# Performance work log

Measured on AMD Instinct MI355X. Metric: run time of the kernel, lower is better.

## Reference

```python
import math
import jax, jax.numpy as jnp
import numpy as np

L, H, D, DFF = 4, 8, 1024, 4096
RGB, AUD = 1024, 128
D_ATT, D_HOP, NCLS = 128, 4, 3862
B, T = 32, 300
EPS = 1e-6


def setup_inputs() -> dict:
    key = jax.random.key(0)
    ks = iter(jax.random.split(key, 40))
    s = 0.02
    p = {
        'padded_frame_rgbs': jax.random.uniform(next(ks), (B, T, RGB), jnp.float32),
        'padded_frame_audios': jax.random.uniform(next(ks), (B, T, AUD), jnp.float32),
        'embed_W': jax.random.normal(next(ks), (RGB + AUD, D), jnp.float32) * s,
        'embed_b': jnp.zeros((D,), jnp.float32),
        'Wq': jax.random.normal(next(ks), (L, D, D), jnp.float32) * s,
        'bq': jnp.zeros((L, D), jnp.float32),
        'Wk': jax.random.normal(next(ks), (L, D, D), jnp.float32) * s,
        'bk': jnp.zeros((L, D), jnp.float32),
        'Wv': jax.random.normal(next(ks), (L, D, D), jnp.float32) * s,
        'bv': jnp.zeros((L, D), jnp.float32),
        'Wo': jax.random.normal(next(ks), (L, D, D), jnp.float32) * s,
        'bo': jnp.zeros((L, D), jnp.float32),
        'ln1_a': jnp.ones((L, D), jnp.float32),
        'ln1_b': jnp.zeros((L, D), jnp.float32),
        'W1f': jax.random.normal(next(ks), (L, D, DFF), jnp.float32) * s,
        'b1f': jnp.zeros((L, DFF), jnp.float32),
        'W2f': jax.random.normal(next(ks), (L, DFF, D), jnp.float32) * s,
        'b2f': jnp.zeros((L, D), jnp.float32),
        'ln2_a': jnp.ones((L, D), jnp.float32),
        'ln2_b': jnp.zeros((L, D), jnp.float32),
        'fn_a': jnp.ones((D,), jnp.float32),
        'fn_b': jnp.zeros((D,), jnp.float32),
        'cw1': jax.random.normal(next(ks), (D, D_ATT), jnp.float32) * s,
        'cb1': jnp.zeros((D_ATT,), jnp.float32),
        'cw2': jax.random.normal(next(ks), (D_ATT, D_HOP), jnp.float32) * s,
        'cb2': jnp.zeros((D_HOP,), jnp.float32),
        'cw3': jax.random.normal(next(ks), (D_HOP * D, DFF), jnp.float32) * s,
        'cb3': jnp.zeros((DFF,), jnp.float32),
        'cw4': jax.random.normal(next(ks), (DFF, NCLS), jnp.float32) * s,
        'cb4': jnp.zeros((NCLS,), jnp.float32),
    }
    return p


def layernorm(x, a, b):
    # torch: a*(x-mean)/(std+eps)+b with unbiased std (ddof=1)
    mean = jnp.mean(x, axis=-1, keepdims=True)
    std = jnp.std(x, axis=-1, keepdims=True, ddof=1)
    return a * (x - mean) / (std + EPS) + b


def positional_encoding(T, D):
    pos = jnp.arange(T, dtype=jnp.float32)[:, None]
    div = jnp.exp(jnp.arange(0, D, 2, dtype=jnp.float32) * (-math.log(10000.0) / D))
    ang = pos * div  # [T, D/2]
    pe = jnp.stack([jnp.sin(ang), jnp.cos(ang)], axis=-1).reshape(T, D)
    return pe


def mha(x, Wq, bq, Wk, bk, Wv, bv, Wo, bo):
    dk = D // H
    q = (x @ Wq + bq).reshape(B, T, H, dk)
    k = (x @ Wk + bk).reshape(B, T, H, dk)
    v = (x @ Wv + bv).reshape(B, T, H, dk)
    scores = jnp.einsum('bthd,bshd->bhts', q, k) / math.sqrt(dk)
    p = jax.nn.softmax(scores, axis=-1)
    o = jnp.einsum('bhts,bshd->bthd', p, v).reshape(B, T, D)
    return o @ Wo + bo


def forward(padded_frame_rgbs, padded_frame_audios, embed_W, embed_b,
            Wq, bq, Wk, bk, Wv, bv, Wo, bo, ln1_a, ln1_b,
            W1f, b1f, W2f, b2f, ln2_a, ln2_b, fn_a, fn_b,
            cw1, cb1, cw2, cb2, cw3, cb3, cw4, cb4):
    feats = jnp.concatenate([padded_frame_rgbs / 255.0,
                             padded_frame_audios / 255.0], axis=2)
    x = (feats @ embed_W + embed_b) * math.sqrt(D)
    x = x + positional_encoding(T, D)[None]
    for i in range(L):
        x = x + mha(layernorm(x, ln1_a[i], ln1_b[i]),
                    Wq[i], bq[i], Wk[i], bk[i], Wv[i], bv[i], Wo[i], bo[i])
        h = layernorm(x, ln2_a[i], ln2_b[i])
        x = x + (jax.nn.relu(h @ W1f[i] + b1f[i]) @ W2f[i] + b2f[i])
    x = layernorm(x, fn_a, fn_b)
    # embedded classifier (multi-hop attention pooling)
    alpha = jnp.tanh(x @ cw1 + cb1) @ cw2 + cb2            # [B, T, D_HOP]
    alpha = jax.nn.softmax(alpha.transpose(0, 2, 1), -1)   # [B, D_HOP, T]
    ws = jnp.einsum('bht,btd->bhd', alpha, x).reshape(B, D_HOP * D)
    out = jnp.tanh(ws @ cw3 + cb3) @ cw4 + cb4             # [B, NCLS]
    return out, alpha


def reference(padded_frame_rgbs, padded_frame_audios, embed_W, embed_b,
              Wq, bq, Wk, bk, Wv, bv, Wo, bo, ln1_a, ln1_b,
              W1f, b1f, W2f, b2f, ln2_a, ln2_b, fn_a, fn_b,
              cw1, cb1, cw2, cb2, cw3, cb3, cw4, cb4):
    return forward(padded_frame_rgbs, padded_frame_audios, embed_W, embed_b,
                   Wq, bq, Wk, bk, Wv, bv, Wo, bo, ln1_a, ln1_b,
                   W1f, b1f, W2f, b2f, ln2_a, ln2_b, fn_a, fn_b,
                   cw1, cb1, cw2, cb2, cw3, cb3, cw4, cb4)
```

## Files before the change

kernel.cpp:

```cpp
#include <hip/hip_runtime.h>
#include <stdint.h>

#define NTOK 9600
#define TT   300
#define DD   1024
#define HH   8
#define DFF  4096
#define FIN  1152
#define DATT 128
#define NCLS 3862
#define TP   320
#define NQT  19

typedef unsigned short u16;
typedef __attribute__((ext_vector_type(8))) short short8;
typedef __attribute__((ext_vector_type(4))) float f32x4;

__device__ __forceinline__ int imin(int a, int b){ return a < b ? a : b; }

__device__ __forceinline__ u16 f2bf(float f){
    union { float f; uint32_t u; } v; v.f = f;
    uint32_t u = v.u;
    return (u16)((u + 0x7fffu + ((u >> 16) & 1u)) >> 16);
}

__device__ __forceinline__ f32x4 mfma16(short8 a, short8 b, f32x4 c){
    return __builtin_amdgcn_mfma_f32_16x16x32_bf16(a, b, c, 0, 0, 0);
}

__device__ __forceinline__ void gll16(const void* g, void* l){
    __builtin_amdgcn_global_load_lds((const __attribute__((address_space(1))) void*)g,
                                     (__attribute__((address_space(3))) void*)l, 16, 0, 0);
}

__global__ void __launch_bounds__(256) pe_kernel(float* __restrict__ pe)
{
    const int i = blockIdx.x * 256 + threadIdx.x;
    if (i >= TT * DD) return;
    const int t = i >> 10, d = i & 1023;
    const float fr = expf(-(float)(d & ~1) * (9.210340371976184f / 1024.0f));
    const float ang = (float)t * fr;
    pe[i] = (d & 1) ? cosf(ang) : sinf(ang);
}

__global__ void __launch_bounds__(256) feats_kernel(const float* __restrict__ rgb,
        const float* __restrict__ aud, u16* __restrict__ out)
{
    const long i = (long)blockIdx.x * 256 + threadIdx.x;
    if (i >= (long)NTOK * FIN) return;
    const int row = (int)(i / FIN), c = (int)(i % FIN);
    const float v = (c < 1024) ? rgb[(size_t)row * 1024 + c] : aud[(size_t)row * 128 + (c - 1024)];
    out[i] = f2bf(v * (1.0f / 255.0f));
}

__global__ void __launch_bounds__(256) wconv_kernel(const float* __restrict__ W,
        u16* __restrict__ Wt, int K, int N)
{
    __shared__ float tile[32][33];
    const int k0 = blockIdx.y * 32, n0 = blockIdx.x * 32;
    const int tx = threadIdx.x, ty = threadIdx.y;
    #pragma unroll
    for (int i = 0; i < 4; ++i) {
        const int k = k0 + ty + i * 8, n = n0 + tx;
        tile[ty + i * 8][tx] = (k < K && n < N) ? W[(size_t)k * N + n] : 0.f;
    }
    __syncthreads();
    #pragma unroll
    for (int i = 0; i < 4; ++i) {
        const int n = n0 + ty + i * 8, k = k0 + tx;
        if (n < N && k < K) Wt[(size_t)n * K + k] = f2bf(tile[tx][ty + i * 8]);
    }
}

__global__ void __launch_bounds__(256) wconv3_kernel(const float* __restrict__ W0,
        const float* __restrict__ W1, const float* __restrict__ W2, u16* __restrict__ Wt)
{
    __shared__ float tile[32][33];
    const float* W = (blockIdx.z == 0) ? W0 : ((blockIdx.z == 1) ? W1 : W2);
    u16* dst = Wt + (size_t)blockIdx.z * DD * DD;
    const int k0 = blockIdx.y * 32, n0 = blockIdx.x * 32;
    const int tx = threadIdx.x, ty = threadIdx.y;
    #pragma unroll
    for (int i = 0; i < 4; ++i)
        tile[ty + i * 8][tx] = W[(size_t)(k0 + ty + i * 8) * DD + n0 + tx];
    __syncthreads();
    #pragma unroll
    for (int i = 0; i < 4; ++i)
        dst[(size_t)(n0 + ty + i * 8) * DD + k0 + tx] = f2bf(tile[tx][ty + i * 8]);
}

__global__ void __launch_bounds__(256) f2bf_kernel(const float* __restrict__ in,
        u16* __restrict__ out, int n)
{
    const int i = blockIdx.x * 256 + threadIdx.x;
    if (i < n) out[i] = f2bf(in[i]);
}

__global__ void __launch_bounds__(256) qkvbias_kernel(const float* __restrict__ bq,
        const float* __restrict__ bk, const float* __restrict__ bv, float* __restrict__ out)
{
    const int i = blockIdx.x * 256 + threadIdx.x;
    if (i >= 4 * 3072) return;
    const int l = i / 3072, c = i % 3072;
    float v;
    if      (c < 1024) v = bq[l * 1024 + c];
    else if (c < 2048) v = bk[l * 1024 + c - 1024];
    else               v = bv[l * 1024 + c - 2048];
    out[i] = v;
}

template<int WF>
__global__ void __launch_bounds__(256) ln_kernel(const float* __restrict__ xin,
        const float* __restrict__ ga, const float* __restrict__ gb,
        u16* __restrict__ ob, float* of)
{
    const int row = blockIdx.x, t = threadIdx.x;
    const float4 xv = *(const float4*)(xin + (size_t)row * 1024 + t * 4);
    float s1 = xv.x + xv.y + xv.z + xv.w;
    float s2 = xv.x * xv.x + xv.y * xv.y + xv.z * xv.z + xv.w * xv.w;
    #pragma unroll
    for (int o = 1; o < 64; o <<= 1) { s1 += __shfl_xor(s1, o); s2 += __shfl_xor(s2, o); }
    __shared__ float r1[4], r2[4];
    const int lane = t & 63, wid = t >> 6;
    if (lane == 0) { r1[wid] = s1; r2[wid] = s2; }
    __syncthreads();
    s1 = r1[0] + r1[1] + r1[2] + r1[3];
    s2 = r2[0] + r2[1] + r2[2] + r2[3];
    const float mean = s1 * (1.0f / 1024.0f);
    const float var  = (s2 - 1024.0f * mean * mean) * (1.0f / 1023.0f);
    const float inv  = 1.0f / (sqrtf(fmaxf(var, 0.f)) + 1e-6f);
    const float4 av  = *(const float4*)(ga + t * 4);
    const float4 bv  = *(const float4*)(gb + t * 4);
    const float y0 = av.x * (xv.x - mean) * inv + bv.x;
    const float y1 = av.y * (xv.y - mean) * inv + bv.y;
    const float y2 = av.z * (xv.z - mean) * inv + bv.z;
    const float y3 = av.w * (xv.w - mean) * inv + bv.w;
    ushort4 o4; o4.x = f2bf(y0); o4.y = f2bf(y1); o4.z = f2bf(y2); o4.w = f2bf(y3);
    *(ushort4*)(ob + (size_t)row * 1024 + t * 4) = o4;
    if (WF) {
        float4 yo; yo.x = y0; yo.y = y1; yo.z = y2; yo.w = y3;
        *(float4*)(of + (size_t)row * 1024 + t * 4) = yo;
    }
}

#define EPI_EMBED        0
#define EPI_QKV          1
#define EPI_B_RELU_BF16  2
#define EPI_B_RES_F32    3
#define EPI_B_TANH_F32   4
#define EPI_ACC_F32      5
#define EPI_PART         6

template<int EPI, int SWZ>
__global__ void __launch_bounds__(256) gemm_k(const u16* __restrict__ A, const u16* __restrict__ Bt,
        const float* __restrict__ bias, const float* extra,
        float* outF, u16* outB, u16* outB2, u16* outB3, int M, int N, int K,
        int lda, int ldb, int kchunk)
{
    __shared__ __align__(16) u16 As[2][4096];
    __shared__ __align__(16) u16 Bs[2][4096];
    const int tid = threadIdx.x;
    int bm, bn;
    if (SWZ) {
        int lin = blockIdx.y * gridDim.x + blockIdx.x;
        const int nwg = gridDim.x * gridDim.y;
        const int cpx = nwg >> 3;
        lin = (lin & 7) * cpx + (lin >> 3);
        bm = lin / gridDim.x;
        bn = lin - bm * gridDim.x;
    } else {
        bm = blockIdx.y; bn = blockIdx.x;
    }
    const int lane = tid & 63, wid = tid >> 6;
    const int lg = lane >> 4, lr = lane & 15;
    const int wr = wid >> 1, wc = wid & 1;

    int koff = 0, Keff = K;
    if (kchunk > 0) { koff = blockIdx.z * kchunk; Keff = kchunk; }

    const int srow = tid >> 2;
    const int skc  = (tid & 3) * 8;
    const u16* ap0 = A  + (size_t)imin(bm * 128 + srow,      M - 1) * lda + skc + koff;
    const u16* ap1 = A  + (size_t)imin(bm * 128 + srow + 64, M - 1) * lda + skc + koff;
    const u16* bp0 = Bt + (size_t)imin(bn * 128 + srow,      N - 1) * ldb + skc + koff;
    const u16* bp1 = Bt + (size_t)imin(bn * 128 + srow + 64, N - 1) * ldb + skc + koff;

    f32x4 acc[4][4] = {};

    auto STAGE = [&](int b, int k0) {
        gll16(ap0 + k0, &As[b][tid * 8]);
        gll16(ap1 + k0, &As[b][2048 + tid * 8]);
        gll16(bp0 + k0, &Bs[b][tid * 8]);
        gll16(bp1 + k0, &Bs[b][2048 + tid * 8]);
    };
    auto COMPUTE = [&](int b) {
        short8 af[4], bf[4];
        #pragma unroll
        for (int m = 0; m < 4; ++m)
            af[m] = *(const short8*)(&As[b][(wr * 64 + m * 16 + lr) * 32 + lg * 8]);
        #pragma unroll
        for (int n = 0; n < 4; ++n)
            bf[n] = *(const short8*)(&Bs[b][(wc * 64 + n * 16 + lr) * 32 + lg * 8]);
        #pragma unroll
        for (int m = 0; m < 4; ++m)
            #pragma unroll
            for (int n = 0; n < 4; ++n)
                acc[m][n] = mfma16(af[m], bf[n], acc[m][n]);
    };

    STAGE(0, 0);
    __syncthreads();
    int cur = 0;
    for (int k0 = 32; k0 < Keff; k0 += 32) {
        STAGE(cur ^ 1, k0);
        COMPUTE(cur);
        __syncthreads();
        cur ^= 1;
    }
    COMPUTE(cur);

    #pragma unroll
    for (int m = 0; m < 4; ++m) {
        const int rb = bm * 128 + wr * 64 + m * 16 + lg * 4;
        #pragma unroll
        for (int n = 0; n < 4; ++n) {
            const int col = bn * 128 + wc * 64 + n * 16 + lr;
            if (col >= N) continue;
            const float bvl = (EPI == EPI_PART || EPI == EPI_ACC_F32) ? 0.f : bias[col];
            #pragma unroll
            for (int j = 0; j < 4; ++j) {
                const int r = rb + j;
                if (r >= M) continue;
                const float v = acc[m][n][j];
                const size_t oi = (size_t)r * N + col;
                if      (EPI == EPI_EMBED)       outF[oi] = (v + bvl) * 32.0f + extra[(size_t)(r % 300) * 1024 + col];
                else if (EPI == EPI_QKV) {
                    const int q = col >> 10, lc = col & 1023;
                    u16* dst = (q == 0) ? outB : ((q == 1) ? outB2 : outB3);
                    dst[(size_t)r * 1024 + lc] = f2bf(v + bvl);
                }
                else if (EPI == EPI_B_RELU_BF16) outB[oi] = f2bf(fmaxf(v + bvl, 0.f));
                else if (EPI == EPI_B_RES_F32)   outF[oi] = v + bvl + extra[oi];
                else if (EPI == EPI_B_TANH_F32)  outF[oi] = tanhf(v + bvl);
                else if (EPI == EPI_ACC_F32)     outF[oi] = v + extra[oi];
                else if (EPI == EPI_PART)        outF[(size_t)blockIdx.z * M * N + oi] = v;
            }
        }
    }
}

template<int EPI>
__global__ void __launch_bounds__(512, 2) gemm_big(const u16* __restrict__ A, const u16* __restrict__ Bt,
        const float* __restrict__ bias, const float* __restrict__ extra,
        float* outF, u16* outB, u16* outB2, u16* outB3,
        int M, int N, int K, int lda, int ldb, int kchunk)
{
    __shared__ __align__(16) u16 LA[2][256 * 32];
    __shared__ __align__(16) u16 LB[2][256 * 32];
    const int tid = threadIdx.x;
    int lin = blockIdx.x;
    const int nwg = gridDim.x;
    if ((nwg & 7) == 0) { const int cpx = nwg >> 3; lin = (lin & 7) * cpx + (lin >> 3); }
    int z = 0;
    if (kchunk > 0) { z = lin & 1; lin >>= 1; }
    const int ntN = N >> 8;
    const int bm = lin / ntN, bn = lin - (lin / ntN) * ntN;
    const int koff = z * kchunk;
    const int Keff = (kchunk > 0) ? kchunk : K;

    const int lane = tid & 63, wid = tid >> 6;
    const int wm = wid >> 2, wn = wid & 3;
    const int lg = lane >> 4, lr = lane & 15;

    const int prow = tid >> 2;
    const int skg  = (((tid & 3) ^ ((tid >> 3) & 3)) * 8);
    const u16* asrc0 = A  + (size_t)imin(bm * 256 + prow,       M - 1) * lda + skg + koff;
    const u16* asrc1 = A  + (size_t)imin(bm * 256 + prow + 128, M - 1) * lda + skg + koff;
    const u16* bsrc0 = Bt + (size_t)(bn * 256 + prow)       * ldb + skg + koff;
    const u16* bsrc1 = Bt + (size_t)(bn * 256 + prow + 128) * ldb + skg + koff;

    auto STAGE = [&](int s, int k0) {
        gll16(asrc0 + k0, &LA[s][tid * 8]);
        gll16(asrc1 + k0, &LA[s][4096 + tid * 8]);
        gll16(bsrc0 + k0, &LB[s][tid * 8]);
        gll16(bsrc1 + k0, &LB[s][4096 + tid * 8]);
    };

    const int kge = (lg ^ ((lr >> 1) & 3)) * 8;
    int aoff[8], boff[4];
    #pragma unroll
    for (int m = 0; m < 8; ++m) aoff[m] = (wm * 128 + m * 16 + lr) * 32 + kge;
    #pragma unroll
    for (int n = 0; n < 4; ++n) boff[n] = (wn * 64 + n * 16 + lr) * 32 + kge;

    f32x4 acc[8][4] = {};
    short8 af[8], bf[4];

    const int nk = Keff >> 5;
    STAGE(0, 0);
    STAGE(1, 32);
    asm volatile("s_waitcnt vmcnt(4)" ::: "memory");
    asm volatile("s_barrier" ::: "memory");
    __builtin_amdgcn_sched_barrier(0);

    auto BODY = [&](int t, int s, bool doStage) {
        #pragma unroll
        for (int m = 0; m < 8; ++m) af[m] = *(const short8*)(&LA[s][aoff[m]]);
        #pragma unroll
        for (int n = 0; n < 4; ++n) bf[n] = *(const short8*)(&LB[s][boff[n]]);
        asm volatile("s_waitcnt lgkmcnt(0)" ::: "memory");
        __builtin_amdgcn_sched_barrier(0);
        __builtin_amdgcn_s_setprio(1);
        #pragma unroll
        for (int m = 0; m < 4; ++m)
            #pragma unroll
            for (int n = 0; n < 4; ++n)
                acc[m][n] = mfma16(af[m], bf[n], acc[m][n]);
        __builtin_amdgcn_s_setprio(0);
        asm volatile("s_barrier" ::: "memory");
        __builtin_amdgcn_sched_barrier(0);
        if (doStage) STAGE(s, (t + 2) * 32);
        __builtin_amdgcn_s_setprio(1);
        #pragma unroll
        for (int m = 4; m < 8; ++m)
            #pragma unroll
            for (int n = 0; n < 4; ++n)
                acc[m][n] = mfma16(af[m], bf[n], acc[m][n]);
        __builtin_amdgcn_s_setprio(0);
    };

    for (int t = 0; t < nk - 2; ++t) {
        BODY(t, t & 1, true);
        asm volatile("s_waitcnt vmcnt(4)" ::: "memory");
        __builtin_amdgcn_sched_barrier(0);
        asm volatile("s_barrier" ::: "memory");
        __builtin_amdgcn_sched_barrier(0);
    }
    BODY(nk - 2, (nk - 2) & 1, false);
    asm volatile("s_waitcnt vmcnt(0)" ::: "memory");
    __builtin_amdgcn_sched_barrier(0);
    asm volatile("s_barrier" ::: "memory");
    __builtin_amdgcn_sched_barrier(0);
    BODY(nk - 1, (nk - 1) & 1, false);

    #pragma unroll
    for (int m = 0; m < 8; ++m) {
        const int rb = bm * 256 + wm * 128 + m * 16 + lg * 4;
        #pragma unroll
        for (int n = 0; n < 4; ++n) {
            const int col = bn * 256 + wn * 64 + n * 16 + lr;
            const float bvl = (EPI == EPI_PART) ? 0.f : bias[col];
            #pragma unroll
            for (int j = 0; j < 4; ++j) {
                const int r = rb + j;
                if (r >= M) continue;
                const float v = acc[m][n][j] + bvl;
                const size_t oi = (size_t)r * N + col;
                if (EPI == EPI_QKV) {
                    const int q = col >> 10, lc = col & 1023;
                    u16* dst = (q == 0) ? outB : ((q == 1) ? outB2 : outB3);
                    dst[(size_t)r * 1024 + lc] = f2bf(v);
                }
                else if (EPI == EPI_B_RELU_BF16) outB[oi] = f2bf(fmaxf(v, 0.f));
                else if (EPI == EPI_B_RES_F32)   outF[oi] = v + extra[oi];
                else if (EPI == EPI_EMBED)       outF[oi] = v * 32.0f + extra[(size_t)(r % 300) * 1024 + col];
                else if (EPI == EPI_PART)        outF[(size_t)z * M * N + oi] = v;
            }
        }
    }
}

template<int TANH>
__global__ void __launch_bounds__(256) redk_kernel(const float* __restrict__ part,
        const float* __restrict__ bias, float* outF, u16* outB, int M, int N, int Z)
{
    const int i = blockIdx.x * 256 + threadIdx.x;
    if (i >= M * N) return;
    const int col = i % N;
    float s = 0.f;
    for (int z = 0; z < Z; ++z) s += part[(size_t)z * M * N + i];
    s += bias[col];
    if (TANH) outB[i] = f2bf(tanhf(s));
    else      outF[i] = s;
}

__global__ void __launch_bounds__(512) attn_scores_kernel(const u16* __restrict__ Qb,
        const u16* __restrict__ Kb, u16* __restrict__ P)
{
    __shared__ __align__(16) u16 Ks[304 * 128];
    __shared__ __align__(16) u16 Ps[8][16][TP];
    const int bh = blockIdx.x, b = bh >> 3, h = bh & 7;
    const int tid = threadIdx.x, lane = tid & 63, wid = tid >> 6;
    const int lg = lane >> 4, lr = lane & 15;

    for (int c = tid; c < 304 * 16; c += 512) {
        const int kv = c >> 4, part = c & 15;
        const int tok = b * 300 + imin(kv, 299);
        const short8 v = *(const short8*)(Kb + (size_t)tok * 1024 + h * 128 + part * 8);
        int byte_ = kv * 256 + part * 16;
        byte_ ^= (kv & 7) << 4;
        *(short8*)((char*)Ks + byte_) = v;
    }
    __syncthreads();

    const float scale = 0.08838834764831845f;
    for (int qt = wid; qt < NQT; qt += 8) {
        f32x4 acc[NQT] = {};
        const int qtok = b * 300 + imin(qt * 16 + lr, 299);
        const u16* qrow = Qb + (size_t)qtok * 1024 + h * 128;
        #pragma unroll
        for (int kk = 0; kk < 4; ++kk) {
            const short8 aq = *(const short8*)(qrow + kk * 32 + lg * 8);
            #pragma unroll
            for (int nt = 0; nt < NQT; ++nt) {
                const int kvrow = nt * 16 + lr;
                int byte_ = kvrow * 256 + kk * 64 + lg * 16;
                byte_ ^= (kvrow & 7) << 4;
                const short8 bk = *(const short8*)((char*)Ks + byte_);
                acc[nt] = mfma16(aq, bk, acc[nt]);
            }
        }
        const int sw = lg << 3;
        #pragma unroll
        for (int j = 0; j < 4; ++j) {
            float vals[NQT];
            float m = -1e30f;
            #pragma unroll
            for (int nt = 0; nt < NQT; ++nt) {
                float s = acc[nt][j] * scale;
                if (nt * 16 + lr >= 300) s = -1e30f;
                vals[nt] = s;
                m = fmaxf(m, s);
            }
            #pragma unroll
            for (int o = 1; o < 16; o <<= 1) m = fmaxf(m, __shfl_xor(m, o));
            float sum = 0.f;
            #pragma unroll
            for (int nt = 0; nt < NQT; ++nt) { const float e = __expf(vals[nt] - m); vals[nt] = e; sum += e; }
            #pragma unroll
            for (int o = 1; o < 16; o <<= 1) sum += __shfl_xor(sum, o);
            const float inv = 1.0f / sum;
            const int row = lg * 4 + j;
            #pragma unroll
            for (int nt = 0; nt < NQT; ++nt) Ps[wid][row][(nt * 16 + lr) ^ sw] = f2bf(vals[nt] * inv);
            Ps[wid][row][(304 + lr) ^ sw] = 0;
        }
        asm volatile("s_waitcnt lgkmcnt(0)" ::: "memory");
        __builtin_amdgcn_sched_barrier(0);
        #pragma unroll
        for (int it = 0; it < 10; ++it) {
            const int idx = it * 64 + lane;
            const int row = idx / 40, c8 = idx - row * 40;
            const int swr = ((row >> 2) & 3) << 3;
            const short8 v8 = *(const short8*)(&Ps[wid][row][(c8 * 8) ^ swr]);
            const int q = qt * 16 + row;
            if (q < 300) *(short8*)(P + ((size_t)bh * 300 + q) * TP + c8 * 8) = v8;
        }
    }
}

__global__ void __launch_bounds__(512) attn_pv_kernel(const u16* __restrict__ P,
        const u16* __restrict__ Vb, u16* __restrict__ O)
{
    __shared__ __align__(16) u16 Vs[128 * TP];
    __shared__ __align__(16) u16 Os[8][16][128];
    const int bh = blockIdx.x, b = bh >> 3, h = bh & 7;
    const int tid = threadIdx.x, lane = tid & 63, wid = tid >> 6;
    const int lg = lane >> 4, lr = lane & 15;

    for (int c = tid; c < 304 * 16; c += 512) {
        const int kv = c >> 4, dp = c & 15;
        const int tok = b * 300 + imin(kv, 299);
        const short8 v = *(const short8*)(Vb + (size_t)tok * 1024 + h * 128 + dp * 8);
        #pragma unroll
        for (int jj = 0; jj < 8; ++jj) {
            const int d = dp * 8 + jj;
            int byte_ = d * (TP * 2) + kv * 2;
            byte_ ^= (d & 7) << 4;
            *(u16*)((char*)Vs + byte_) = (u16)v[jj];
        }
    }
    for (int c = tid; c < 128 * 16; c += 512) {
        const int d = c >> 4, kv = 304 + (c & 15);
        int byte_ = d * (TP * 2) + kv * 2;
        byte_ ^= (d & 7) << 4;
        *(u16*)((char*)Vs + byte_) = 0;
    }
    __syncthreads();

    for (int qt = wid; qt < NQT; qt += 8) {
        f32x4 acc[8] = {};
        const int q = imin(qt * 16 + lr, 299);
        const u16* prow = P + ((size_t)bh * 300 + q) * TP;
        #pragma unroll
        for (int kk = 0; kk < 10; ++kk) {
            const short8 ap = *(const short8*)(prow + kk * 32 + lg * 8);
            #pragma unroll
            for (int nt = 0; nt < 8; ++nt) {
                const int d = nt * 16 + lr;
                int byte_ = d * (TP * 2) + kk * 64 + lg * 16;
                byte_ ^= (d & 7) << 4;
                const short8 bv8 = *(const short8*)((char*)Vs + byte_);
                acc[nt] = mfma16(ap, bv8, acc[nt]);
            }
        }
        const int sw = lg << 3;
        #pragma unroll
        for (int nt = 0; nt < 8; ++nt)
            #pragma unroll
            for (int j = 0; j < 4; ++j)
                Os[wid][lg * 4 + j][(nt * 16 + lr) ^ sw] = f2bf(acc[nt][j]);
        asm volatile("s_waitcnt lgkmcnt(0)" ::: "memory");
        __builtin_amdgcn_sched_barrier(0);
        #pragma unroll
        for (int it = 0; it < 4; ++it) {
            const int idx = it * 64 + lane;
            const int row = idx >> 4, c8 = idx & 15;
            const int swr = ((row >> 2) & 3) << 3;
            const short8 v8 = *(const short8*)(&Os[wid][row][(c8 * 8) ^ swr]);
            const int qq = qt * 16 + row;
            if (qq < 300)
                *(short8*)(O + ((size_t)(b * 300 + qq)) * 1024 + h * 128 + c8 * 8) = v8;
        }
    }
}

__global__ void __launch_bounds__(256) logits_kernel(const float* __restrict__ a1,
        const float* __restrict__ cw2, const float* __restrict__ cb2, float* __restrict__ out)
{
    const int tok = blockIdx.x * 4 + (threadIdx.x >> 6);
    const int lane = threadIdx.x & 63;
    if (tok >= NTOK) return;
    const float v0 = a1[(size_t)tok * 128 + lane];
    const float v1 = a1[(size_t)tok * 128 + 64 + lane];
    #pragma unroll
    for (int hp = 0; hp < 4; ++hp) {
        float s = v0 * cw2[lane * 4 + hp] + v1 * cw2[(64 + lane) * 4 + hp];
        #pragma unroll
        for (int o = 1; o < 64; o <<= 1) s += __shfl_xor(s, o);
        if (lane == 0) out[(size_t)tok * 4 + hp] = s + cb2[hp];
    }
}

__global__ void __launch_bounds__(512) softmaxT_kernel(const float* __restrict__ lgt,
        float* __restrict__ alpha, float* __restrict__ outAlpha)
{
    const int bh = blockIdx.x;
    const int b = bh >> 2, hp = bh & 3;
    const int t = threadIdx.x;
    const float v = (t < 300) ? lgt[((size_t)(b * 300 + t)) * 4 + hp] : -1e30f;
    float m = v;
    #pragma unroll
    for (int o = 1; o < 64; o <<= 1) m = fmaxf(m, __shfl_xor(m, o));
    __shared__ float rm[8], rs[8];
    const int lane = t & 63, wid = t >> 6;
    if (lane == 0) rm[wid] = m;
    __syncthreads();
    m = rm[0];
    #pragma unroll
    for (int i = 1; i < 8; ++i) m = fmaxf(m, rm[i]);
    const float e = (t < 300) ? __expf(v - m) : 0.f;
    float s = e;
    #pragma unroll
    for (int o = 1; o < 64; o <<= 1) s += __shfl_xor(s, o);
    if (lane == 0) rs[wid] = s;
    __syncthreads();
    s = rs[0] + rs[1] + rs[2] + rs[3] + rs[4] + rs[5] + rs[6] + rs[7];
    if (t < 300) {
        const float a = e / s;
        alpha[(size_t)bh * 300 + t] = a;
        outAlpha[(size_t)bh * 300 + t] = a;
    }
}

__global__ void __launch_bounds__(256) pool_kernel(const float* __restrict__ alpha,
        const float* __restrict__ xln, float* __restrict__ wsp)
{
    const int bh = blockIdx.x, b = bh >> 2;
    const int d = blockIdx.y * 256 + threadIdx.x;
    const float* xp = xln + (size_t)b * 300 * 1024 + d;
    const float* al = alpha + (size_t)bh * 300;
    float acc = 0.f;
    for (int t = 0; t < 300; ++t) acc += al[t] * xp[(size_t)t * 1024];
    wsp[(size_t)bh * 1024 + d] = acc;
}

extern "C" void kernel_launch(void* const* d_in, const int* in_sizes, int n_in,
                              void* d_out, int out_size, void* d_ws, size_t ws_size,
                              hipStream_t stream)
{
    const float* rgb     = (const float*)d_in[0];
    const float* aud     = (const float*)d_in[1];
    const float* embed_W = (const float*)d_in[2];
    const float* embed_b = (const float*)d_in[3];
    const float* Wq      = (const float*)d_in[4];
    const float* bq      = (const float*)d_in[5];
    const float* Wk      = (const float*)d_in[6];
    const float* bk      = (const float*)d_in[7];
    const float* Wv      = (const float*)d_in[8];
    const float* bv      = (const float*)d_in[9];
    const float* Wo      = (const float*)d_in[10];
    const float* bo      = (const float*)d_in[11];
    const float* ln1_a   = (const float*)d_in[12];
    const float* ln1_b   = (const float*)d_in[13];
    const float* W1f     = (const float*)d_in[14];
    const float* b1f     = (const float*)d_in[15];
    const float* W2f     = (const float*)d_in[16];
    const float* b2f     = (const float*)d_in[17];
    const float* ln2_a   = (const float*)d_in[18];
    const float* ln2_b   = (const float*)d_in[19];
    const float* fn_a    = (const float*)d_in[20];
    const float* fn_b    = (const float*)d_in[21];
    const float* cw1     = (const float*)d_in[22];
    const float* cb1     = (const float*)d_in[23];
    const float* cw2     = (const float*)d_in[24];
    const float* cb2     = (const float*)d_in[25];
    const float* cw3     = (const float*)d_in[26];
    const float* cb3     = (const float*)d_in[27];
    const float* cw4     = (const float*)d_in[28];
    const float* cb4     = (const float*)d_in[29];

    const bool bigS = ws_size >= ((size_t)238 << 20);
    const size_t Ssz = bigS ? (size_t)NTOK * DFF * 2 : (size_t)256 * 300 * TP * 2;

    char* base = (char*)d_ws;
    size_t off = 0;
    auto alloc = [&](size_t bytes) -> char* {
        char* p = base + off; off += (bytes + 255) & ~(size_t)255; return p; };

    float* x    = (float*)alloc((size_t)NTOK * DD * 4);
    float* pe   = (float*)alloc((size_t)TT * DD * 4);
    u16*  hbuf  = (u16*) alloc((size_t)NTOK * DD * 2);
    u16*  Qb    = (u16*) alloc((size_t)NTOK * DD * 2);
    u16*  Kb    = (u16*) alloc((size_t)NTOK * DD * 2);
    u16*  Vb    = (u16*) alloc((size_t)NTOK * DD * 2);
    u16*  S     = (u16*) alloc(Ssz);
    float* lgts = (float*)alloc((size_t)NTOK * 4 * 4);
    float* alph = (float*)alloc((size_t)128 * 300 * 4);
    float* wsp  = (float*)alloc((size_t)32 * 4096 * 4);
    u16*  wsb   = (u16*) alloc((size_t)32 * 4096 * 2);
    u16*  t3b   = (u16*) alloc((size_t)32 * 4096 * 2);
    float* bqkv = (float*)alloc((size_t)4 * 3072 * 4);
    u16*  eWt   = (u16*) alloc((size_t)1024 * 1152 * 2);
    u16*  WqkvT = (u16*) alloc((size_t)3 * 1024 * 1024 * 2);
    u16*  WoT   = (u16*) alloc((size_t)1024 * 1024 * 2);
    u16*  W1T   = (u16*) alloc((size_t)DFF * DD * 2);
    u16*  W2T   = (u16*) alloc((size_t)DD * DFF * 2);
    u16*  c1T   = (u16*) alloc((size_t)128 * 1024 * 2);
    if (off > ws_size) return;

    u16*  featsb = S;
    u16*  pbuf   = S;
    u16*  midc   = S;
    u16*  Ob     = hbuf;
    float* xln   = (float*)Qb;
    u16*  xlnb   = Vb;
    float* a1    = (float*)S;
    u16*  c3T    = (u16*)x;
    u16*  c4T    = S;
    float* part  = (float*)hbuf;
    float* outv     = (float*)d_out;
    float* outAlpha = outv + (size_t)32 * NCLS;

    const dim3 blk(256);

    pe_kernel<<<(TT * DD + 255) / 256, blk, 0, stream>>>(pe);
    feats_kernel<<<(int)(((size_t)NTOK * FIN + 255) / 256), blk, 0, stream>>>(rgb, aud, featsb);
    qkvbias_kernel<<<(4 * 3072 + 255) / 256, blk, 0, stream>>>(bq, bk, bv, bqkv);

    auto wconv = [&](const float* W, u16* Wt, int K, int N) {
        dim3 g((N + 31) / 32, (K + 31) / 32);
        wconv_kernel<<<g, dim3(32, 8), 0, stream>>>(W, Wt, K, N);
    };
    wconv(embed_W, eWt, FIN, DD);
    wconv(cw1, c1T, DD, DATT);

    gemm_k<EPI_EMBED, 1><<<dim3(8, 75), blk, 0, stream>>>(featsb, eWt, embed_b, pe, x,
            nullptr, nullptr, nullptr, NTOK, DD, FIN, FIN, FIN, 0);

    for (int i = 0; i < 4; ++i) {
        wconv3_kernel<<<dim3(32, 32, 3), dim3(32, 8), 0, stream>>>(
                Wq + (size_t)i * DD * DD, Wk + (size_t)i * DD * DD, Wv + (size_t)i * DD * DD, WqkvT);
        wconv(Wo  + (size_t)i * DD * DD,  WoT, DD, DD);
        wconv(W1f + (size_t)i * DD * DFF, W1T, DD, DFF);
        wconv(W2f + (size_t)i * DFF * DD, W2T, DFF, DD);

        ln_kernel<0><<<NTOK, blk, 0, stream>>>(x, ln1_a + (size_t)i * DD, ln1_b + (size_t)i * DD, hbuf, nullptr);
        gemm_big<EPI_QKV><<<456, dim3(512), 0, stream>>>(hbuf, WqkvT, bqkv + (size_t)i * 3072, nullptr,
                nullptr, Qb, Kb, Vb, NTOK, 3072, DD, DD, DD, 0);
        attn_scores_kernel<<<256, dim3(512), 0, stream>>>(Qb, Kb, pbuf);
        attn_pv_kernel<<<256, dim3(512), 0, stream>>>(pbuf, Vb, Ob);
        gemm_k<EPI_B_RES_F32, 1><<<dim3(8, 75), blk, 0, stream>>>(Ob, WoT, bo + (size_t)i * DD, x, x,
                nullptr, nullptr, nullptr, NTOK, DD, DD, DD, DD, 0);
        ln_kernel<0><<<NTOK, blk, 0, stream>>>(x, ln2_a + (size_t)i * DD, ln2_b + (size_t)i * DD, hbuf, nullptr);
        if (bigS) {
            gemm_big<EPI_B_RELU_BF16><<<608, dim3(512), 0, stream>>>(hbuf, W1T, b1f + (size_t)i * DFF,
                    nullptr, nullptr, midc, nullptr, nullptr, NTOK, DFF, DD, DD, DD, 0);
            gemm_k<EPI_B_RES_F32, 1><<<dim3(8, 75), blk, 0, stream>>>(midc, W2T, b2f + (size_t)i * DD,
                    x, x, nullptr, nullptr, nullptr, NTOK, DD, DFF, DFF, DFF, 0);
        } else {
            for (int h = 0; h < 2; ++h) {
                gemm_big<EPI_B_RELU_BF16><<<304, dim3(512), 0, stream>>>(hbuf, W1T + (size_t)h * 2048 * DD,
                        b1f + (size_t)i * DFF + h * 2048, nullptr, nullptr, midc, nullptr, nullptr,
                        NTOK, 2048, DD, DD, DD, 0);
                if (h == 0)
                    gemm_k<EPI_B_RES_F32, 1><<<dim3(8, 75), blk, 0, stream>>>(midc, W2T + (size_t)h * 2048,
                            b2f + (size_t)i * DD, x, x, nullptr, nullptr, nullptr, NTOK, DD, 2048, 2048, DFF, 0);
                else
                    gemm_k<EPI_ACC_F32, 1><<<dim3(8, 75), blk, 0, stream>>>(midc, W2T + (size_t)h * 2048,
                            b2f + (size_t)i * DD, x, x, nullptr, nullptr, nullptr, NTOK, DD, 2048, 2048, DFF, 0);
            }
        }
    }

    ln_kernel<1><<<NTOK, blk, 0, stream>>>(x, fn_a, fn_b, xlnb, xln);
    wconv(cw3, c3T, 4096, DFF);
    gemm_k<EPI_B_TANH_F32, 0><<<dim3(1, 75), blk, 0, stream>>>(xlnb, c1T, cb1, nullptr, a1,
            nullptr, nullptr, nullptr, NTOK, DATT, DD, DD, DD, 0);
    logits_kernel<<<2400, blk, 0, stream>>>(a1, cw2, cb2, lgts);
    wconv(cw4, c4T, DFF, NCLS);
    softmaxT_kernel<<<128, dim3(512), 0, stream>>>(lgts, alph, outAlpha);
    pool_kernel<<<dim3(128, 4), blk, 0, stream>>>(alph, xln, wsp);
    f2bf_kernel<<<(32 * 4096 + 255) / 256, blk, 0, stream>>>(wsp, wsb, 32 * 4096);

    gemm_k<EPI_PART, 0><<<dim3(32, 1, 8), blk, 0, stream>>>(wsb, c3T, nullptr, nullptr, part,
            nullptr, nullptr, nullptr, 32, 4096, 4096, 4096, 4096, 512);
    redk_kernel<1><<<(32 * 4096 + 255) / 256, blk, 0, stream>>>(part, cb3, nullptr, t3b, 32, 4096, 8);
    gemm_k<EPI_PART, 0><<<dim3(31, 1, 8), blk, 0, stream>>>(t3b, c4T, nullptr, nullptr, part,
            nullptr, nullptr, nullptr, 32, NCLS, 4096, 4096, 4096, 512);
    redk_kernel<0><<<(32 * NCLS + 255) / 256, blk, 0, stream>>>(part, cb4, outv, nullptr, 32, NCLS, 8);
}
```

Baseline: 2.346 ms.

## Add 128x128-tile double-buffered MFMA GEMM for N=1024 projections

Introduces gemm_mid, a 128x128 tile bf16 MFMA GEMM with direct global-to-LDS loads, double buffering, swizzled LDS layout, split MFMA phases with priority hints and XCD-aware block remapping. It replaces the 8x75-grid gemm_k for the embedding, attention output projection and FFN down-projection (bigS path). The aim is better occupancy and wave count for N=1024 outputs (600 blocks instead of 600 larger tiles with fewer waves). The tradeoff is a smaller tile with lower arithmetic intensity per block.

```diff
diff --git a/kernel.cpp b/kernel.cpp
--- a/kernel.cpp
+++ b/kernel.cpp
@@ -365,6 +365,115 @@
                 else if (EPI == EPI_B_RES_F32)   outF[oi] = v + extra[oi];
                 else if (EPI == EPI_EMBED)       outF[oi] = v * 32.0f + extra[(size_t)(r % 300) * 1024 + col];
                 else if (EPI == EPI_PART)        outF[(size_t)z * M * N + oi] = v;
+            }
+        }
+    }
+}
+
+template<int EPI>
+__global__ void __launch_bounds__(256, 3) gemm_mid(const u16* __restrict__ A, const u16* __restrict__ Bt,
+        const float* __restrict__ bias, const float* __restrict__ extra,
+        float* outF, u16* outB, int M, int N, int K, int lda, int ldb)
+{
+    __shared__ __align__(16) u16 LA[2][128 * 32];
+    __shared__ __align__(16) u16 LB[2][128 * 32];
+    const int tid = threadIdx.x;
+    int lin = blockIdx.x;
+    const int nwg = gridDim.x;
+    if ((nwg & 7) == 0) { const int cpx = nwg >> 3; lin = (lin & 7) * cpx + (lin >> 3); }
+    const int ntN = N >> 7;
+    const int bm = lin / ntN, bn = lin - (lin / ntN) * ntN;
+
+    const int lane = tid & 63, wid = tid >> 6;
+    const int wr = wid >> 1, wc = wid & 1;
+    const int lg = lane >> 4, lr = lane & 15;
+
+    const int prow = tid >> 2;
+    const int skg  = (((tid & 3) ^ ((tid >> 3) & 3)) * 8);
+    const u16* asrc0 = A  + (size_t)imin(bm * 128 + prow,      M - 1) * lda + skg;
+    const u16* asrc1 = A  + (size_t)imin(bm * 128 + prow + 64, M - 1) * lda + skg;
+    const u16* bsrc0 = Bt + (size_t)(bn * 128 + prow)      * ldb + skg;
+    const u16* bsrc1 = Bt + (size_t)(bn * 128 + prow + 64) * ldb + skg;
+
+    auto STAGE = [&](int s, int k0) {
+        gll16(asrc0 + k0, &LA[s][tid * 8]);
+        gll16(asrc1 + k0, &LA[s][2048 + tid * 8]);
+        gll16(bsrc0 + k0, &LB[s][tid * 8]);
+        gll16(bsrc1 + k0, &LB[s][2048 + tid * 8]);
+    };
+
+    const int kge = (lg ^ ((lr >> 1) & 3)) * 8;
+    int aoff[4], boff[4];
+    #pragma unroll
+    for (int m = 0; m < 4; ++m) aoff[m] = (wr * 64 + m * 16 + lr) * 32 + kge;
+    #pragma unroll
+    for (int n = 0; n < 4; ++n) boff[n] = (wc * 64 + n * 16 + lr) * 32 + kge;
+
+    f32x4 acc[4][4] = {};
+    short8 af[4], bf[4];
+
+    const int nk = K >> 5;
+    STAGE(0, 0);
+    STAGE(1, 32);
+    asm volatile("s_waitcnt vmcnt(4)" ::: "memory");
+    asm volatile("s_barrier" ::: "memory");
+    __builtin_amdgcn_sched_barrier(0);
+
+    auto BODY = [&](int t, int s, bool doStage) {
+        #pragma unroll
+        for (int m = 0; m < 4; ++m) af[m] = *(const short8*)(&LA[s][aoff[m]]);
+        #pragma unroll
+        for (int n = 0; n < 4; ++n) bf[n] = *(const short8*)(&LB[s][boff[n]]);
+        asm volatile("s_waitcnt lgkmcnt(0)" ::: "memory");
+        __builtin_amdgcn_sched_barrier(0);
+        __builtin_amdgcn_s_setprio(1);
+        #pragma unroll
+        for (int m = 0; m < 2; ++m)
+            #pragma unroll
+            for (int n = 0; n < 4; ++n)
+                acc[m][n] = mfma16(af[m], bf[n], acc[m][n]);
+        __builtin_amdgcn_s_setprio(0);
+        asm volatile("s_barrier" ::: "memory");
+        __builtin_amdgcn_sched_barrier(0);
+        if (doStage) STAGE(s, (t + 2) * 32);
+        __builtin_amdgcn_s_setprio(1);
+        #pragma unroll
+        for (int m = 2; m < 4; ++m)
+            #pragma unroll
+            for (int n = 0; n < 4; ++n)
+                acc[m][n] = mfma16(af[m], bf[n], acc[m][n]);
+        __builtin_amdgcn_s_setprio(0);
+    };
+
+    for (int t = 0; t < nk - 2; ++t) {
+        BODY(t, t & 1, true);
+        asm volatile("s_waitcnt vmcnt(4)" ::: "memory");
+        __builtin_amdgcn_sched_barrier(0);
+        asm volatile("s_barrier" ::: "memory");
+        __builtin_amdgcn_sched_barrier(0);
+    }
+    BODY(nk - 2, (nk - 2) & 1, false);
+    asm volatile("s_waitcnt vmcnt(0)" ::: "memory");
+    __builtin_amdgcn_sched_barrier(0);
+    asm volatile("s_barrier" ::: "memory");
+    __builtin_amdgcn_sched_barrier(0);
+    BODY(nk - 1, (nk - 1) & 1, false);
+
+    #pragma unroll
+    for (int m = 0; m < 4; ++m) {
+        const int rb = bm * 128 + wr * 64 + m * 16 + lg * 4;
+        #pragma unroll
+        for (int n = 0; n < 4; ++n) {
+            const int col = bn * 128 + wc * 64 + n * 16 + lr;
+            const float bvl = bias[col];
+            #pragma unroll
+            for (int j = 0; j < 4; ++j) {
+                const int r = rb + j;
+                if (r >= M) continue;
+                const float v = acc[m][n][j] + bvl;
+                const size_t oi = (size_t)r * N + col;
+                if      (EPI == EPI_B_RES_F32) outF[oi] = v + extra[oi];
+                else if (EPI == EPI_EMBED)     outF[oi] = v * 32.0f + extra[(size_t)(r % 300) * 1024 + col];
             }
         }
     }
@@ -675,8 +784,8 @@
     wconv(embed_W, eWt, FIN, DD);
     wconv(cw1, c1T, DD, DATT);
 
-    gemm_k<EPI_EMBED, 1><<<dim3(8, 75), blk, 0, stream>>>(featsb, eWt, embed_b, pe, x,
-            nullptr, nullptr, nullptr, NTOK, DD, FIN, FIN, FIN, 0);
+    gemm_mid<EPI_EMBED><<<600, blk, 0, stream>>>(featsb, eWt, embed_b, pe, x, nullptr,
+            NTOK, DD, FIN, FIN, FIN);
 
     for (int i = 0; i < 4; ++i) {
         wconv3_kernel<<<dim3(32, 32, 3), dim3(32, 8), 0, stream>>>(
@@ -690,14 +799,14 @@
                 nullptr, Qb, Kb, Vb, NTOK, 3072, DD, DD, DD, 0);
         attn_scores_kernel<<<256, dim3(512), 0, stream>>>(Qb, Kb, pbuf);
         attn_pv_kernel<<<256, dim3(512), 0, stream>>>(pbuf, Vb, Ob);
-        gemm_k<EPI_B_RES_F32, 1><<<dim3(8, 75), blk, 0, stream>>>(Ob, WoT, bo + (size_t)i * DD, x, x,
-                nullptr, nullptr, nullptr, NTOK, DD, DD, DD, DD, 0);
+        gemm_mid<EPI_B_RES_F32><<<600, blk, 0, stream>>>(Ob, WoT, bo + (size_t)i * DD, x, x, nullptr,
+                NTOK, DD, DD, DD, DD);
         ln_kernel<0><<<NTOK, blk, 0, stream>>>(x, ln2_a + (size_t)i * DD, ln2_b + (size_t)i * DD, hbuf, nullptr);
         if (bigS) {
             gemm_big<EPI_B_RELU_BF16><<<608, dim3(512), 0, stream>>>(hbuf, W1T, b1f + (size_t)i * DFF,
                     nullptr, nullptr, midc, nullptr, nullptr, NTOK, DFF, DD, DD, DD, 0);
-            gemm_k<EPI_B_RES_F32, 1><<<dim3(8, 75), blk, 0, stream>>>(midc, W2T, b2f + (size_t)i * DD,
-                    x, x, nullptr, nullptr, nullptr, NTOK, DD, DFF, DFF, DFF, 0);
+            gemm_mid<EPI_B_RES_F32><<<600, blk, 0, stream>>>(midc, W2T, b2f + (size_t)i * DD, x, x, nullptr,
+                    NTOK, DD, DFF, DFF, DFF);
         } else {
             for (int h = 0; h < 2; ++h) {
                 gemm_big<EPI_B_RELU_BF16><<<304, dim3(512), 0, stream>>>(hbuf, W1T + (size_t)h * 2048 * DD,
```

After: 2.160 ms. -7.9%, faster.

## Replace 256x256 GEMM kernel with 128x128 tile kernel across all main GEMMs

Applied to the files above, without the earlier changes.

The 512-thread 256x256-tile GEMM is replaced by a 256-thread 128x128-tile kernel, launched with 3 blocks per CU, and used for the embed, QKV, output-projection, FFN and classifier GEMMs. Smaller tiles give many more workgroups (600–2400), which improves wave balance across CUs, especially for the N=1024 GEMMs that previously ran on a 600-block generic kernel. The LDS wait is also moved after the first half of the MFMAs so that LDS reads overlap with compute. In exchange, each tile reuses global loads less, so more memory traffic goes to L2/HBM per FLOP.

```diff
diff --git a/kernel.cpp b/kernel.cpp
--- a/kernel.cpp
+++ b/kernel.cpp
@@ -250,53 +250,49 @@
 }
 
 template<int EPI>
-__global__ void __launch_bounds__(512, 2) gemm_big(const u16* __restrict__ A, const u16* __restrict__ Bt,
+__global__ void __launch_bounds__(256, 3) gemm_mid(const u16* __restrict__ A, const u16* __restrict__ Bt,
         const float* __restrict__ bias, const float* __restrict__ extra,
         float* outF, u16* outB, u16* outB2, u16* outB3,
-        int M, int N, int K, int lda, int ldb, int kchunk)
-{
-    __shared__ __align__(16) u16 LA[2][256 * 32];
-    __shared__ __align__(16) u16 LB[2][256 * 32];
+        int M, int N, int K, int lda, int ldb)
+{
+    __shared__ __align__(16) u16 LA[2][128 * 32];
+    __shared__ __align__(16) u16 LB[2][128 * 32];
     const int tid = threadIdx.x;
     int lin = blockIdx.x;
     const int nwg = gridDim.x;
     if ((nwg & 7) == 0) { const int cpx = nwg >> 3; lin = (lin & 7) * cpx + (lin >> 3); }
-    int z = 0;
-    if (kchunk > 0) { z = lin & 1; lin >>= 1; }
-    const int ntN = N >> 8;
+    const int ntN = N >> 7;
     const int bm = lin / ntN, bn = lin - (lin / ntN) * ntN;
-    const int koff = z * kchunk;
-    const int Keff = (kchunk > 0) ? kchunk : K;
 
     const int lane = tid & 63, wid = tid >> 6;
-    const int wm = wid >> 2, wn = wid & 3;
+    const int wr = wid >> 1, wc = wid & 1;
     const int lg = lane >> 4, lr = lane & 15;
 
     const int prow = tid >> 2;
     const int skg  = (((tid & 3) ^ ((tid >> 3) & 3)) * 8);
-    const u16* asrc0 = A  + (size_t)imin(bm * 256 + prow,       M - 1) * lda + skg + koff;
-    const u16* asrc1 = A  + (size_t)imin(bm * 256 + prow + 128, M - 1) * lda + skg + koff;
-    const u16* bsrc0 = Bt + (size_t)(bn * 256 + prow)       * ldb + skg + koff;
-    const u16* bsrc1 = Bt + (size_t)(bn * 256 + prow + 128) * ldb + skg + koff;
+    const u16* asrc0 = A  + (size_t)imin(bm * 128 + prow,      M - 1) * lda + skg;
+    const u16* asrc1 = A  + (size_t)imin(bm * 128 + prow + 64, M - 1) * lda + skg;
+    const u16* bsrc0 = Bt + (size_t)(bn * 128 + prow)      * ldb + skg;
+    const u16* bsrc1 = Bt + (size_t)(bn * 128 + prow + 64) * ldb + skg;
 
     auto STAGE = [&](int s, int k0) {
         gll16(asrc0 + k0, &LA[s][tid * 8]);
-        gll16(asrc1 + k0, &LA[s][4096 + tid * 8]);
+        gll16(asrc1 + k0, &LA[s][2048 + tid * 8]);
         gll16(bsrc0 + k0, &LB[s][tid * 8]);
-        gll16(bsrc1 + k0, &LB[s][4096 + tid * 8]);
+        gll16(bsrc1 + k0, &LB[s][2048 + tid * 8]);
     };
 
     const int kge = (lg ^ ((lr >> 1) & 3)) * 8;
-    int aoff[8], boff[4];
-    #pragma unroll
-    for (int m = 0; m < 8; ++m) aoff[m] = (wm * 128 + m * 16 + lr) * 32 + kge;
-    #pragma unroll
-    for (int n = 0; n < 4; ++n) boff[n] = (wn * 64 + n * 16 + lr) * 32 + kge;
-
-    f32x4 acc[8][4] = {};
-    short8 af[8], bf[4];
-
-    const int nk = Keff >> 5;
+    int aoff[4], boff[4];
+    #pragma unroll
+    for (int m = 0; m < 4; ++m) aoff[m] = (wr * 64 + m * 16 + lr) * 32 + kge;
+    #pragma unroll
+    for (int n = 0; n < 4; ++n) boff[n] = (wc * 64 + n * 16 + lr) * 32 + kge;
+
+    f32x4 acc[4][4] = {};
+    short8 af[4], bf[4];
+
+    const int nk = K >> 5;
     STAGE(0, 0);
     STAGE(1, 32);
     asm volatile("s_waitcnt vmcnt(4)" ::: "memory");
@@ -305,24 +301,24 @@
 
     auto BODY = [&](int t, int s, bool doStage) {
         #pragma unroll
-        for (int m = 0; m < 8; ++m) af[m] = *(const short8*)(&LA[s][aoff[m]]);
+        for (int m = 0; m < 4; ++m) af[m] = *(const short8*)(&LA[s][aoff[m]]);
         #pragma unroll
         for (int n = 0; n < 4; ++n) bf[n] = *(const short8*)(&LB[s][boff[n]]);
-        asm volatile("s_waitcnt lgkmcnt(0)" ::: "memory");
-        __builtin_amdgcn_sched_barrier(0);
         __builtin_amdgcn_s_setprio(1);
         #pragma unroll
-        for (int m = 0; m < 4; ++m)
+        for (int m = 0; m < 2; ++m)
             #pragma unroll
             for (int n = 0; n < 4; ++n)
                 acc[m][n] = mfma16(af[m], bf[n], acc[m][n]);
         __builtin_amdgcn_s_setprio(0);
+        asm volatile("s_waitcnt lgkmcnt(0)" ::: "memory");
+        __builtin_amdgcn_sched_barrier(0);
         asm volatile("s_barrier" ::: "memory");
         __builtin_amdgcn_sched_barrier(0);
         if (doStage) STAGE(s, (t + 2) * 32);
         __builtin_amdgcn_s_setprio(1);
         #pragma unroll
-        for (int m = 4; m < 8; ++m)
+        for (int m = 2; m < 4; ++m)
             #pragma unroll
             for (int n = 0; n < 4; ++n)
                 acc[m][n] = mfma16(af[m], bf[n], acc[m][n]);
@@ -344,27 +340,27 @@
     BODY(nk - 1, (nk - 1) & 1, false);
 
     #pragma unroll
-    for (int m = 0; m < 8; ++m) {
-        const int rb = bm * 256 + wm * 128 + m * 16 + lg * 4;
+    for (int m = 0; m < 4; ++m) {
+        const int rb = bm * 128 + wr * 64 + m * 16 + lg * 4;
         #pragma unroll
         for (int n = 0; n < 4; ++n) {
-            const int col = bn * 256 + wn * 64 + n * 16 + lr;
-            const float bvl = (EPI == EPI_PART) ? 0.f : bias[col];
+            const int col = bn * 128 + wc * 64 + n * 16 + lr;
+            const float bvl = bias[col];
             #pragma unroll
             for (int j = 0; j < 4; ++j) {
                 const int r = rb + j;
                 if (r >= M) continue;
                 const float v = acc[m][n][j] + bvl;
                 const size_t oi = (size_t)r * N + col;
-                if (EPI == EPI_QKV) {
+                if      (EPI == EPI_B_RES_F32)   outF[oi] = v + extra[oi];
+                else if (EPI == EPI_EMBED)       outF[oi] = v * 32.0f + extra[(size_t)(r % 300) * 1024 + col];
+                else if (EPI == EPI_B_RELU_BF16) outB[oi] = f2bf(fmaxf(v, 0.f));
+                else if (EPI == EPI_B_TANH_F32)  outF[oi] = tanhf(v);
+                else if (EPI == EPI_QKV) {
                     const int q = col >> 10, lc = col & 1023;
                     u16* dst = (q == 0) ? outB : ((q == 1) ? outB2 : outB3);
                     dst[(size_t)r * 1024 + lc] = f2bf(v);
                 }
-                else if (EPI == EPI_B_RELU_BF16) outB[oi] = f2bf(fmaxf(v, 0.f));
-                else if (EPI == EPI_B_RES_F32)   outF[oi] = v + extra[oi];
-                else if (EPI == EPI_EMBED)       outF[oi] = v * 32.0f + extra[(size_t)(r % 300) * 1024 + col];
-                else if (EPI == EPI_PART)        outF[(size_t)z * M * N + oi] = v;
             }
         }
     }
@@ -675,8 +671,8 @@
     wconv(embed_W, eWt, FIN, DD);
     wconv(cw1, c1T, DD, DATT);
 
-    gemm_k<EPI_EMBED, 1><<<dim3(8, 75), blk, 0, stream>>>(featsb, eWt, embed_b, pe, x,
-            nullptr, nullptr, nullptr, NTOK, DD, FIN, FIN, FIN, 0);
+    gemm_mid<EPI_EMBED><<<600, blk, 0, stream>>>(featsb, eWt, embed_b, pe, x,
+            nullptr, nullptr, nullptr, NTOK, DD, FIN, FIN, FIN);
 
     for (int i = 0; i < 4; ++i) {
         wconv3_kernel<<<dim3(32, 32, 3), dim3(32, 8), 0, stream>>>(
@@ -686,23 +682,23 @@
         wconv(W2f + (size_t)i * DFF * DD, W2T, DFF, DD);
 
         ln_kernel<0><<<NTOK, blk, 0, stream>>>(x, ln1_a + (size_t)i * DD, ln1_b + (size_t)i * DD, hbuf, nullptr);
-        gemm_big<EPI_QKV><<<456, dim3(512), 0, stream>>>(hbuf, WqkvT, bqkv + (size_t)i * 3072, nullptr,
-                nullptr, Qb, Kb, Vb, NTOK, 3072, DD, DD, DD, 0);
+        gemm_mid<EPI_QKV><<<1800, blk, 0, stream>>>(hbuf, WqkvT, bqkv + (size_t)i * 3072, nullptr,
+                nullptr, Qb, Kb, Vb, NTOK, 3072, DD, DD, DD);
         attn_scores_kernel<<<256, dim3(512), 0, stream>>>(Qb, Kb, pbuf);
         attn_pv_kernel<<<256, dim3(512), 0, stream>>>(pbuf, Vb, Ob);
-        gemm_k<EPI_B_RES_F32, 1><<<dim3(8, 75), blk, 0, stream>>>(Ob, WoT, bo + (size_t)i * DD, x, x,
-                nullptr, nullptr, nullptr, NTOK, DD, DD, DD, DD, 0);
+        gemm_mid<EPI_B_RES_F32><<<600, blk, 0, stream>>>(Ob, WoT, bo + (size_t)i * DD, x, x,
+                nullptr, nullptr, nullptr, NTOK, DD, DD, DD, DD);
         ln_kernel<0><<<NTOK, blk, 0, stream>>>(x, ln2_a + (size_t)i * DD, ln2_b + (size_t)i * DD, hbuf, nullptr);
         if (bigS) {
-            gemm_big<EPI_B_RELU_BF16><<<608, dim3(512), 0, stream>>>(hbuf, W1T, b1f + (size_t)i * DFF,
-                    nullptr, nullptr, midc, nullptr, nullptr, NTOK, DFF, DD, DD, DD, 0);
-            gemm_k<EPI_B_RES_F32, 1><<<dim3(8, 75), blk, 0, stream>>>(midc, W2T, b2f + (size_t)i * DD,
-                    x, x, nullptr, nullptr, nullptr, NTOK, DD, DFF, DFF, DFF, 0);
+            gemm_mid<EPI_B_RELU_BF16><<<2400, blk, 0, stream>>>(hbuf, W1T, b1f + (size_t)i * DFF,
+                    nullptr, nullptr, midc, nullptr, nullptr, NTOK, DFF, DD, DD, DD);
+            gemm_mid<EPI_B_RES_F32><<<600, blk, 0, stream>>>(midc, W2T, b2f + (size_t)i * DD, x, x,
+                    nullptr, nullptr, nullptr, NTOK, DD, DFF, DFF, DFF);
         } else {
             for (int h = 0; h < 2; ++h) {
-                gemm_big<EPI_B_RELU_BF16><<<304, dim3(512), 0, stream>>>(hbuf, W1T + (size_t)h * 2048 * DD,
+                gemm_mid<EPI_B_RELU_BF16><<<1200, blk, 0, stream>>>(hbuf, W1T + (size_t)h * 2048 * DD,
                         b1f + (size_t)i * DFF + h * 2048, nullptr, nullptr, midc, nullptr, nullptr,
-                        NTOK, 2048, DD, DD, DD, 0);
+                        NTOK, 2048, DD, DD, DD);
                 if (h == 0)
                     gemm_k<EPI_B_RES_F32, 1><<<dim3(8, 75), blk, 0, stream>>>(midc, W2T + (size_t)h * 2048,
                             b2f + (size_t)i * DD, x, x, nullptr, nullptr, nullptr, NTOK, DD, 2048, 2048, DFF, 0);
@@ -715,8 +711,8 @@
 
     ln_kernel<1><<<NTOK, blk, 0, stream>>>(x, fn_a, fn_b, xlnb, xln);
     wconv(cw3, c3T, 4096, DFF);
-    gemm_k<EPI_B_TANH_F32, 0><<<dim3(1, 75), blk, 0, stream>>>(xlnb, c1T, cb1, nullptr, a1,
-            nullptr, nullptr, nullptr, NTOK, DATT, DD, DD, DD, 0);
+    gemm_mid<EPI_B_TANH_F32><<<75, blk, 0, stream>>>(xlnb, c1T, cb1, nullptr, a1,
+            nullptr, nullptr, nullptr, NTOK, DATT, DD, DD, DD);
     logits_kernel<<<2400, blk, 0, stream>>>(a1, cw2, cb2, lgts);
     wconv(cw4, c4T, DFF, NCLS);
     softmaxT_kernel<<<128, dim3(512), 0, stream>>>(lgts, alph, outAlpha);
```

Result: faster. 2.083 ms (-11.2%).
